# Kernel optimization log

Hardware: AMD Instinct MI355X
Metric: run time of the kernel (lower is better)

The kernel has to match this reference:

```python
import jax, jax.numpy as jnp
import numpy as np

B, T, D_IN, D_OUT = 64, 1024, 512, 512


def setup_inputs() -> dict:
    key = jax.random.key(0)
    k_x, k_w, k_wr = jax.random.split(key, 3)
    x = jax.random.normal(k_x, (B, T, D_IN), dtype=jnp.float32)
    # glorot_uniform for W
    limit = np.sqrt(6.0 / (D_IN + D_OUT)).astype(np.float32)
    W = jax.random.uniform(k_w, (D_IN, D_OUT), dtype=jnp.float32, minval=-limit, maxval=limit)
    # orthogonal for W_recurrent
    a = jax.random.normal(k_wr, (D_OUT, D_OUT), dtype=jnp.float32)
    q, r = jnp.linalg.qr(a)
    W_recurrent = q * jnp.sign(jnp.diag(r))[None, :]
    b = jnp.zeros((D_OUT,), dtype=jnp.float32)
    return {"x": x, "W": W, "W_recurrent": W_recurrent, "b": b}


def reference(x, W, W_recurrent, b):
    # x: [B, T, D_in]; sequential tanh RNN; return last hidden state [B, D_out]
    x_t = jnp.transpose(x, (1, 0, 2))  # [T, B, D_in]
    h0 = jnp.zeros((x.shape[0], W.shape[1]), dtype=x.dtype)

    def step(h, xt):
        h_new = jnp.tanh(xt @ W + h @ W_recurrent + b)
        return h_new, None

    h_last, _ = jax.lax.scan(step, h0, x_t)
    return h_last
```

## Files before the change

kernel.cpp:

```cpp
#include <hip/hip_runtime.h>
#include <math.h>

#define BATCH   64
#define TSTEPS  1024
#define DIN     512
#define DH      512
#define MDIM    (BATCH * TSTEPS)
#define MB      16

#define BLDS_W   15360
#define BLDS_ALL 122880
#define K2_LDS   (BLDS_ALL + 2 * 16384)

typedef _Float16 f16x8 __attribute__((ext_vector_type(8)));
typedef float    f32x4 __attribute__((ext_vector_type(4)));

__device__ inline unsigned short f2h_bits(float x) {
    _Float16 h = (_Float16)x;
    return __builtin_bit_cast(unsigned short, h);
}
__device__ inline float ftanh(float x) {
    float e = __builtin_amdgcn_exp2f(x * 2.88539008177792681472f);
    return 1.0f - 2.0f * __builtin_amdgcn_rcpf(e + 1.0f);
}

__global__ __launch_bounds__(256) void convert_x(const float* __restrict__ x,
                                                 _Float16* __restrict__ xh,
                                                 int nvec) {
    int i = blockIdx.x * blockDim.x + threadIdx.x;
    int stride = gridDim.x * blockDim.x;
    for (; i < nvec; i += stride) {
        const float4* p = (const float4*)x + 2 * (size_t)i;
        float4 a = p[0], b = p[1];
        f16x8 o = { (_Float16)a.x, (_Float16)a.y, (_Float16)a.z, (_Float16)a.w,
                    (_Float16)b.x, (_Float16)b.y, (_Float16)b.z, (_Float16)b.w };
        ((f16x8*)xh)[i] = o;
    }
}

__global__ __launch_bounds__(256) void transpose_w(const float* __restrict__ W,
                                                   _Float16* __restrict__ Wt) {
    __shared__ float tile[64][65];
    const int t  = threadIdx.x;
    const int c  = t & 63;
    const int r0 = t >> 6;
    const int bn = blockIdx.x & 7;
    const int bk = blockIdx.x >> 3;
    const int k0 = bk * 64, n0 = bn * 64;
    #pragma unroll
    for (int i = 0; i < 16; ++i)
        tile[r0 + 4 * i][c] = W[(size_t)(k0 + r0 + 4 * i) * DH + n0 + c];
    __syncthreads();
    #pragma unroll
    for (int i = 0; i < 16; ++i)
        Wt[(size_t)(n0 + r0 + 4 * i) * DIN + k0 + c] = (_Float16)tile[c][r0 + 4 * i];
}

__global__ __launch_bounds__(512) void pack_b3(const _Float16* __restrict__ Wrt,
                                               _Float16* __restrict__ Wrp) {
    const int i  = blockIdx.x * 512 + threadIdx.x;
    const int wv = i >> 10;
    const int c  = (i >> 6) & 15;
    const int l  = i & 63;
    const int col = wv * 64 + 48 + (l & 15);
    const int k0  = c * 32 + (l >> 4) * 8;
    ((f16x8*)Wrp)[i] = *(const f16x8*)&Wrt[(size_t)col * DIN + k0];
}

__global__ __launch_bounds__(256) void gemm_xw_mfma(const _Float16* __restrict__ Xh,
                                                    const _Float16* __restrict__ Wt,
                                                    const float* __restrict__ bias,
                                                    float* __restrict__ XW) {
    __shared__ __align__(16) _Float16 Ah[128][32];
    __shared__ __align__(16) _Float16 Bh[128][32];

    const int tid  = threadIdx.x;
    const int wv   = tid >> 6;
    const int lane = tid & 63;
    const int bn   = blockIdx.x & 3;
    const int bm   = blockIdx.x >> 2;
    const int m0   = bm * 128;
    const int n0   = bn * 128;

    const int mbase = (wv >> 1) * 64;
    const int nbase = (wv & 1) * 64;
    const int fr    = lane & 15;
    const int fq    = lane >> 4;

    f32x4 acc[4][4];
    #pragma unroll
    for (int i = 0; i < 4; ++i)
        #pragma unroll
        for (int j = 0; j < 4; ++j)
            acc[i][j] = (f32x4){0.f, 0.f, 0.f, 0.f};

    for (int kc = 0; kc < DIN / 32; ++kc) {
        const int k0 = kc * 32;
#if __has_builtin(__builtin_amdgcn_global_load_lds)
        #pragma unroll
        for (int q = 0; q < 2; ++q) {
            const int rb = wv * 2 + q;
            const int gr = (rb * 16) + (lane >> 2);
            const int gc = (lane & 3) * 8;
            const _Float16* ga = Xh + (size_t)(m0 + gr) * DIN + k0 + gc;
            const _Float16* gb = Wt + (size_t)(n0 + gr) * DIN + k0 + gc;
            __builtin_amdgcn_global_load_lds(
                (const __attribute__((address_space(1))) void*)ga,
                (__attribute__((address_space(3))) void*)&Ah[rb * 16][0], 16, 0, 0);
            __builtin_amdgcn_global_load_lds(
                (const __attribute__((address_space(1))) void*)gb,
                (__attribute__((address_space(3))) void*)&Bh[rb * 16][0], 16, 0, 0);
        }
#else
        #pragma unroll
        for (int q = 0; q < 2; ++q) {
            const int h0 = (q * 256 + tid) * 8;
            const int row = h0 >> 5, col = h0 & 31;
            *((uint4*)Ah + (q * 256 + tid)) =
                *(const uint4*)(Xh + (size_t)(m0 + row) * DIN + k0 + col);
            *((uint4*)Bh + (q * 256 + tid)) =
                *(const uint4*)(Wt + (size_t)(n0 + row) * DIN + k0 + col);
        }
#endif
        __syncthreads();

        f16x8 af[4], bf[4];
        #pragma unroll
        for (int mt = 0; mt < 4; ++mt)
            af[mt] = *(const f16x8*)&Ah[mbase + mt * 16 + fr][fq * 8];
        #pragma unroll
        for (int nt = 0; nt < 4; ++nt)
            bf[nt] = *(const f16x8*)&Bh[nbase + nt * 16 + fr][fq * 8];
        #pragma unroll
        for (int mt = 0; mt < 4; ++mt)
            #pragma unroll
            for (int nt = 0; nt < 4; ++nt)
                acc[mt][nt] = __builtin_amdgcn_mfma_f32_16x16x32_f16(
                    af[mt], bf[nt], acc[mt][nt], 0, 0, 0);
        __syncthreads();
    }

    #pragma unroll
    for (int nt = 0; nt < 4; ++nt) {
        const int col = n0 + nbase + nt * 16 + fr;
        const float bvl = bias[col];
        #pragma unroll
        for (int mt = 0; mt < 4; ++mt) {
            #pragma unroll
            for (int r = 0; r < 4; ++r) {
                const int row = m0 + mbase + mt * 16 + fq * 4 + r;
                XW[(size_t)row * DH + col] = acc[mt][nt][r] + bvl;
            }
        }
    }
}

__global__ __launch_bounds__(256) void gemm_xw(const float* __restrict__ X,
                                               const float* __restrict__ W,
                                               const float* __restrict__ bias,
                                               float* __restrict__ XW) {
    __shared__ float As[16][68];
    __shared__ float Bs[16][68];
    const int tid = threadIdx.x;
    const int bx  = blockIdx.x & 7;
    const int by  = blockIdx.x >> 3;
    const int m0  = by * 64, n0 = bx * 64;
    const int ty = tid >> 4, tx = tid & 15;
    const int arow = tid >> 2, akq = (tid & 3) * 4;
    const int brow = tid >> 4, bcq = (tid & 15) * 4;
    float acc[4][4] = {{0.f}};
    for (int k0 = 0; k0 < DIN; k0 += 16) {
        float4 av = *(const float4*)&X[(size_t)(m0 + arow) * DIN + k0 + akq];
        float4 bv = *(const float4*)&W[(size_t)(k0 + brow) * DH + n0 + bcq];
        __syncthreads();
        As[akq + 0][arow] = av.x; As[akq + 1][arow] = av.y;
        As[akq + 2][arow] = av.z; As[akq + 3][arow] = av.w;
        *(float4*)&Bs[brow][bcq] = bv;
        __syncthreads();
        #pragma unroll
        for (int k = 0; k < 16; ++k) {
            float4 a = *(const float4*)&As[k][ty * 4];
            float4 b = *(const float4*)&Bs[k][tx * 4];
            float ar[4] = {a.x, a.y, a.z, a.w};
            float br[4] = {b.x, b.y, b.z, b.w};
            #pragma unroll
            for (int i = 0; i < 4; ++i)
                #pragma unroll
                for (int j = 0; j < 4; ++j)
                    acc[i][j] = fmaf(ar[i], br[j], acc[i][j]);
        }
    }
    float4 bv = *(const float4*)&bias[n0 + tx * 4];
    const float br[4] = {bv.x, bv.y, bv.z, bv.w};
    #pragma unroll
    for (int i = 0; i < 4; ++i) {
        float4 o;
        o.x = acc[i][0] + br[0]; o.y = acc[i][1] + br[1];
        o.z = acc[i][2] + br[2]; o.w = acc[i][3] + br[3];
        *(float4*)&XW[(size_t)(m0 + ty * 4 + i) * DH + n0 + tx * 4] = o;
    }
}

__global__ __launch_bounds__(512, 1) void rnn_scan_lds(const float* __restrict__ XW,
                                                       const _Float16* __restrict__ Wrt,
                                                       const _Float16* __restrict__ Wrp,
                                                       float* __restrict__ Hout) {
    extern __shared__ __align__(16) char lds[];
    char* bwl   = lds;
    char* Hbase = lds + BLDS_ALL;

    const int tid  = threadIdx.x;
    const int wv   = tid >> 6;
    const int lane = tid & 63;
    const int fr   = lane & 15;
    const int fq   = lane >> 4;
    const int b0   = blockIdx.x * MB;

    for (int i = tid; i < 4096; i += 512) ((unsigned int*)Hbase)[i] = 0u;

    f16x8 breg[3][16];
    #pragma unroll
    for (int s = 0; s < 3; ++s) {
        const int col = wv * 64 + s * 16 + fr;
        #pragma unroll
        for (int c = 0; c < 16; ++c)
            breg[s][c] = *(const f16x8*)&Wrt[(size_t)col * DH + c * 32 + fq * 8];
    }

    {
        const f16x8* src = (const f16x8*)Wrp + wv * 1024 + lane;
        char* dst = bwl + wv * BLDS_W + lane * 16;
        #pragma unroll
        for (int c = 0; c < 15; ++c)
            *(f16x8*)(dst + c * 1024) = src[c * 64];
    }
    __syncthreads();

    const float* xbase = XW + (size_t)(b0 + fq * 4) * TSTEPS * DH + wv * 64 + fr;
    const f16x8* b15   = (const f16x8*)Wrp + wv * 1024 + 15 * 64 + lane;
    const char*  bw    = bwl + wv * BLDS_W + lane * 16;

    const int ebase = wv * 1024 + ((fr >> 3) * 16 + fq * 4) * 8 + (fr & 7);

    #pragma unroll 1
    for (int t = 0; t < TSTEPS; ++t) {
        const char* Hr = Hbase + ((t & 1) << 14);
        char*       Hw = Hbase + (((t + 1) & 1) << 14);

        int toff = 0;
        asm volatile("" : "+v"(toff));
        f16x8 bs = b15[toff];

        float xv[4][4];
        #pragma unroll
        for (int s = 0; s < 4; ++s)
            #pragma unroll
            for (int r = 0; r < 4; ++r)
                xv[s][r] = xbase[(size_t)r * TSTEPS * DH + (size_t)t * DH + s * 16];

        f32x4 cc[4];
        #pragma unroll
        for (int s = 0; s < 4; ++s) cc[s] = (f32x4){0.f, 0.f, 0.f, 0.f};

        #pragma unroll
        for (int c = 0; c < 15; ++c) {
            f16x8 af = *(const f16x8*)(Hr + c * 1024 + lane * 16);
            f16x8 bf = *(const f16x8*)(bw + c * 1024);
            cc[0] = __builtin_amdgcn_mfma_f32_16x16x32_f16(af, breg[0][c], cc[0], 0, 0, 0);
            cc[1] = __builtin_amdgcn_mfma_f32_16x16x32_f16(af, breg[1][c], cc[1], 0, 0, 0);
            cc[2] = __builtin_amdgcn_mfma_f32_16x16x32_f16(af, breg[2][c], cc[2], 0, 0, 0);
            cc[3] = __builtin_amdgcn_mfma_f32_16x16x32_f16(af, bf,         cc[3], 0, 0, 0);
        }
        {
            f16x8 af = *(const f16x8*)(Hr + 15 * 1024 + lane * 16);
            cc[0] = __builtin_amdgcn_mfma_f32_16x16x32_f16(af, breg[0][15], cc[0], 0, 0, 0);
            cc[1] = __builtin_amdgcn_mfma_f32_16x16x32_f16(af, breg[1][15], cc[1], 0, 0, 0);
            cc[2] = __builtin_amdgcn_mfma_f32_16x16x32_f16(af, breg[2][15], cc[2], 0, 0, 0);
            cc[3] = __builtin_amdgcn_mfma_f32_16x16x32_f16(af, bs,          cc[3], 0, 0, 0);
        }

        #pragma unroll
        for (int s = 0; s < 4; ++s) {
            #pragma unroll
            for (int r = 0; r < 4; ++r) {
                const float a = cc[s][r] + xv[s][r];
                ((unsigned short*)Hw)[ebase + (s >> 1) * 512 + (s & 1) * 256 + r * 8] =
                    f2h_bits(ftanh(a));
            }
        }
        __syncthreads();
    }

    {
        const int m  = tid >> 5;
        const int cg = tid & 31;
        const int cb = cg * 16;
        const int c  = cg >> 1;
        const int fb = (cg & 1) * 2;
        const char* Hb0 = Hbase;
        #pragma unroll
        for (int g = 0; g < 2; ++g) {
            f16x8 v = *(const f16x8*)(Hb0 + c * 1024 + ((fb + g) * 16 + m) * 16);
            float4 o0 = { (float)v[0], (float)v[1], (float)v[2], (float)v[3] };
            float4 o1 = { (float)v[4], (float)v[5], (float)v[6], (float)v[7] };
            *(float4*)&Hout[(size_t)(b0 + m) * DH + cb + g * 8]     = o0;
            *(float4*)&Hout[(size_t)(b0 + m) * DH + cb + g * 8 + 4] = o1;
        }
    }
}

extern "C" void kernel_launch(void* const* d_in, const int* in_sizes, int n_in,
                              void* d_out, int out_size, void* d_ws, size_t ws_size,
                              hipStream_t stream) {
    const float* x  = (const float*)d_in[0];
    const float* W  = (const float*)d_in[1];
    const float* Wr = (const float*)d_in[2];
    const float* bv = (const float*)d_in[3];
    float* out = (float*)d_out;

    const size_t XW_BYTES  = (size_t)MDIM * DH * sizeof(float);
    const size_t WRT_BYTES = (size_t)DH * DH * sizeof(_Float16);
    const size_t WRP_BYTES = (size_t)8 * 16 * 64 * 8 * sizeof(_Float16);
    const size_t XH_BYTES  = (size_t)MDIM * DIN * sizeof(_Float16);
    const size_t WT_BYTES  = (size_t)DIN * DH * sizeof(_Float16);

    const size_t SCAN_MIN = XW_BYTES + WRT_BYTES + WRP_BYTES;
    if (ws_size < SCAN_MIN) return;

    char* base = (char*)d_ws;
    float*    xw  = (float*)base;
    _Float16* wrt = (_Float16*)(base + XW_BYTES);
    _Float16* wrp = (_Float16*)(base + XW_BYTES + WRT_BYTES);

    hipFuncSetAttribute((const void*)rnn_scan_lds,
                        hipFuncAttributeMaxDynamicSharedMemorySize, K2_LDS);

    transpose_w<<<dim3(64), dim3(256), 0, stream>>>(Wr, wrt);
    pack_b3<<<dim3(16), dim3(512), 0, stream>>>(wrt, wrp);

    if (ws_size >= SCAN_MIN + XH_BYTES + WT_BYTES) {
        _Float16* xh = (_Float16*)(base + SCAN_MIN);
        _Float16* wt = (_Float16*)(base + SCAN_MIN + XH_BYTES);
        convert_x<<<dim3(2048), dim3(256), 0, stream>>>(x, xh, MDIM * DIN / 8);
        transpose_w<<<dim3(64), dim3(256), 0, stream>>>(W, wt);
        gemm_xw_mfma<<<dim3((MDIM / 128) * (DH / 128)), dim3(256), 0, stream>>>(
            xh, wt, bv, xw);
    } else {
        gemm_xw<<<dim3((MDIM / 64) * (DH / 64)), dim3(256), 0, stream>>>(x, W, bv, xw);
    }

    rnn_scan_lds<<<dim3(BATCH / MB), dim3(512), K2_LDS, stream>>>(xw, wrt, wrp, out);
}
```

Measured before the change: 1.977 ms.

## Add 1024-thread scan kernel holding all recurrent weights in registers

Adds a recurrent scan kernel that runs 16 waves per block, each owning 32 output columns. The full recurrent weight matrix therefore fits in registers, so the per-step weight reads from LDS and the extra global fetch of the old kernel are no longer needed. At runtime the host checks whether the new kernel spills to scratch and falls back to the old kernel if it does. The trade-off is more waves taking part in each per-step barrier and heavier register pressure per thread.

```diff
diff --git a/kernel.cpp b/kernel.cpp
--- a/kernel.cpp
+++ b/kernel.cpp
@@ -201,6 +201,82 @@
     }
 }
 
+__global__ __launch_bounds__(1024, 1) void rnn_scan_wide(const float* __restrict__ XW,
+                                                         const _Float16* __restrict__ Wrt,
+                                                         float* __restrict__ Hout) {
+    __shared__ __align__(16) _Float16 H[2][8192];
+
+    const int tid  = threadIdx.x;
+    const int wv   = tid >> 6;
+    const int lane = tid & 63;
+    const int fr   = lane & 15;
+    const int fq   = lane >> 4;
+    const int b0   = blockIdx.x * MB;
+
+    for (int i = tid; i < 4096; i += 1024) ((unsigned int*)H[0])[i] = 0u;
+
+    f16x8 breg[2][16];
+    #pragma unroll
+    for (int s = 0; s < 2; ++s) {
+        const int col = wv * 32 + s * 16 + fr;
+        #pragma unroll
+        for (int c = 0; c < 16; ++c)
+            breg[s][c] = *(const f16x8*)&Wrt[(size_t)col * DH + c * 32 + fq * 8];
+    }
+    __syncthreads();
+
+    const float* xbase = XW + (size_t)(b0 + fq * 4) * TSTEPS * DH + wv * 32 + fr;
+
+    const int ebase = wv * 512 + ((fr >> 3) * 16 + fq * 4) * 8 + (fr & 7);
+
+    #pragma unroll 1
+    for (int t = 0; t < TSTEPS; ++t) {
+        const char* Hr = (const char*)H[t & 1];
+        char*       Hw = (char*)H[(t + 1) & 1];
+
+        float xv[2][4];
+        #pragma unroll
+        for (int s = 0; s < 2; ++s)
+            #pragma unroll
+            for (int r = 0; r < 4; ++r)
+                xv[s][r] = xbase[(size_t)r * TSTEPS * DH + (size_t)t * DH + s * 16];
+
+        f32x4 cc[2];
+        cc[0] = (f32x4){0.f, 0.f, 0.f, 0.f};
+        cc[1] = (f32x4){0.f, 0.f, 0.f, 0.f};
+
+        #pragma unroll
+        for (int c = 0; c < 16; ++c) {
+            f16x8 af = *(const f16x8*)(Hr + c * 1024 + lane * 16);
+            cc[0] = __builtin_amdgcn_mfma_f32_16x16x32_f16(af, breg[0][c], cc[0], 0, 0, 0);
+            cc[1] = __builtin_amdgcn_mfma_f32_16x16x32_f16(af, breg[1][c], cc[1], 0, 0, 0);
+        }
+
+        #pragma unroll
+        for (int s = 0; s < 2; ++s) {
+            #pragma unroll
+            for (int r = 0; r < 4; ++r) {
+                const float a = cc[s][r] + xv[s][r];
+                ((unsigned short*)Hw)[ebase + s * 256 + r * 8] = f2h_bits(ftanh(a));
+            }
+        }
+        __syncthreads();
+    }
+
+    {
+        const int m   = tid >> 6;
+        const int cg  = tid & 63;
+        const int c   = cg >> 2;
+        const int fqp = cg & 3;
+        const char* Hb0 = (const char*)H[0];
+        f16x8 v = *(const f16x8*)(Hb0 + c * 1024 + (fqp * 16 + m) * 16);
+        float4 o0 = { (float)v[0], (float)v[1], (float)v[2], (float)v[3] };
+        float4 o1 = { (float)v[4], (float)v[5], (float)v[6], (float)v[7] };
+        *(float4*)&Hout[(size_t)(b0 + m) * DH + cg * 8]     = o0;
+        *(float4*)&Hout[(size_t)(b0 + m) * DH + cg * 8 + 4] = o1;
+    }
+}
+
 __global__ __launch_bounds__(512, 1) void rnn_scan_lds(const float* __restrict__ XW,
                                                        const _Float16* __restrict__ Wrt,
                                                        const _Float16* __restrict__ Wrp,
@@ -226,7 +302,6 @@
         for (int c = 0; c < 16; ++c)
             breg[s][c] = *(const f16x8*)&Wrt[(size_t)col * DH + c * 32 + fq * 8];
     }
-
     {
         const f16x8* src = (const f16x8*)Wrp + wv * 1024 + lane;
         char* dst = bwl + wv * BLDS_W + lane * 16;
@@ -331,6 +406,16 @@
     float*    xw  = (float*)base;
     _Float16* wrt = (_Float16*)(base + XW_BYTES);
     _Float16* wrp = (_Float16*)(base + XW_BYTES + WRT_BYTES);
+
+    static int use_wide = -1;
+    if (use_wide < 0) {
+        hipFuncAttributes fa;
+        if (hipFuncGetAttributes(&fa, (const void*)rnn_scan_wide) == hipSuccess &&
+            fa.localSizeBytes == 0)
+            use_wide = 1;
+        else
+            use_wide = 0;
+    }
 
     hipFuncSetAttribute((const void*)rnn_scan_lds,
                         hipFuncAttributeMaxDynamicSharedMemorySize, K2_LDS);
@@ -349,5 +434,8 @@
         gemm_xw<<<dim3((MDIM / 64) * (DH / 64)), dim3(256), 0, stream>>>(x, W, bv, xw);
     }
 
-    rnn_scan_lds<<<dim3(BATCH / MB), dim3(512), K2_LDS, stream>>>(xw, wrt, wrp, out);
-}
+    if (use_wide)
+        rnn_scan_wide<<<dim3(BATCH / MB), dim3(1024), 0, stream>>>(xw, wrt, out);
+    else
+        rnn_scan_lds<<<dim3(BATCH / MB), dim3(512), K2_LDS, stream>>>(xw, wrt, wrp, out);
+}
```

Result: no change. 1.975 ms (-0.1%).
